# Performance work log

Measured on AMD Instinct MI355X. Metric: run time of the kernel, lower is better.

## Reference

```python
import jax, jax.numpy as jnp
import numpy as np

E = 1024   # embedding_dim
A = 1024   # attention_dim
H = 16     # num_heads
D = A // H # head_dim


def setup_inputs() -> dict:
    key = jax.random.key(0)
    ks = jax.random.split(key, 9)
    s = 1.0 / np.sqrt(E)
    so = 1.0 / np.sqrt(A)
    return {
        "x": jax.random.normal(ks[0], (2, 2048, E), dtype=jnp.float32),
        "Wq": jax.random.uniform(ks[1], (E, A), jnp.float32, -s, s),
        "bq": jax.random.uniform(ks[2], (A,), jnp.float32, -s, s),
        "Wk": jax.random.uniform(ks[3], (E, A), jnp.float32, -s, s),
        "bk": jax.random.uniform(ks[4], (A,), jnp.float32, -s, s),
        "Wv": jax.random.uniform(ks[5], (E, A), jnp.float32, -s, s),
        "bv": jax.random.uniform(ks[6], (A,), jnp.float32, -s, s),
        "Wo": jax.random.uniform(ks[7], (A, E), jnp.float32, -so, so),
        "bo": jax.random.uniform(ks[8], (E,), jnp.float32, -so, so),
    }


def reference(x, Wq, bq, Wk, bk, Wv, bv, Wo, bo):
    B, S, _ = x.shape
    # projections -> [B, H, S, D]
    def split_heads(t):
        return t.reshape(B, S, H, D).transpose(0, 2, 1, 3)
    Q = split_heads(x @ Wq + bq)
    K = split_heads(x @ Wk + bk)
    V = split_heads(x @ Wv + bv)
    scores = jnp.einsum("bhqd,bhkd->bhqk", Q, K) / jnp.sqrt(jnp.float32(D))
    causal = jnp.tril(jnp.ones((S, S), dtype=bool))
    scores = jnp.where(causal, scores, -jnp.inf)
    attn = jax.nn.softmax(scores, axis=-1)  # dropout p=0 (eval/deterministic)
    ctx = jnp.einsum("bhqk,bhkd->bhqd", attn, V)
    ctx = ctx.transpose(0, 2, 1, 3).reshape(B, S, A)
    out = ctx @ Wo + bo
    return (out, attn)
```

## Files before the change

### kernel.cpp

```cpp
#include <hip/hip_runtime.h>
#include <cstddef>

typedef __bf16 bf16_t;
typedef __attribute__((ext_vector_type(8))) __bf16 bf16x8;
typedef __attribute__((ext_vector_type(4))) float f32x4;

#define BATCH 2
#define SEQ   2048
#define EMB   1024
#define ADIM  1024
#define NHEAD 16
#define HDIM  64
#define MROWS 4096

__device__ inline unsigned short f2bf(float f) {
    bf16_t b = (bf16_t)f;
    return __builtin_bit_cast(unsigned short, b);
}

__global__ __launch_bounds__(256) void convert_x_kernel(
    const float* __restrict__ in, unsigned short* __restrict__ out, int n8)
{
    int i = blockIdx.x * 256 + threadIdx.x;
    if (i >= n8) return;
    const float4* p = (const float4*)(in + (size_t)i * 8);
    float4 a = p[0], b = p[1];
    unsigned int w0 = f2bf(a.x) | ((unsigned)f2bf(a.y) << 16);
    unsigned int w1 = f2bf(a.z) | ((unsigned)f2bf(a.w) << 16);
    unsigned int w2 = f2bf(b.x) | ((unsigned)f2bf(b.y) << 16);
    unsigned int w3 = f2bf(b.z) | ((unsigned)f2bf(b.w) << 16);
    uint4 v = {w0, w1, w2, w3};
    *(uint4*)(out + (size_t)i * 8) = v;
}

__global__ __launch_bounds__(256) void transpose_w_kernel(
    const float* __restrict__ Wq, const float* __restrict__ Wk,
    const float* __restrict__ Wv, const float* __restrict__ Wo,
    unsigned short* __restrict__ Wt_qkv, unsigned short* __restrict__ Wt_o)
{
    __shared__ float tile[64][65];
    const int m = blockIdx.z;
    const float* W = (m == 0) ? Wq : (m == 1) ? Wk : (m == 2) ? Wv : Wo;
    unsigned short* dst = (m < 3) ? (Wt_qkv + (size_t)m * 1024 * 1024) : Wt_o;
    const int r0 = blockIdx.y * 64, c0 = blockIdx.x * 64;
    const int t = threadIdx.x;
    const int r = t >> 2, c4 = (t & 3) * 16;
    #pragma unroll
    for (int j = 0; j < 16; j += 4) {
        float4 v = *(const float4*)(W + (size_t)(r0 + r) * 1024 + c0 + c4 + j);
        tile[r][c4 + j + 0] = v.x;
        tile[r][c4 + j + 1] = v.y;
        tile[r][c4 + j + 2] = v.z;
        tile[r][c4 + j + 3] = v.w;
    }
    __syncthreads();
    const int oc = t >> 2, ch = (t & 3) * 16;
    unsigned int ww[8];
    #pragma unroll
    for (int j = 0; j < 16; j += 2)
        ww[j >> 1] = f2bf(tile[ch + j][oc]) | ((unsigned)f2bf(tile[ch + j + 1][oc]) << 16);
    unsigned short* o = dst + (size_t)(c0 + oc) * 1024 + r0 + ch;
    *(uint4*)(o) = *(uint4*)&ww[0];
    *(uint4*)(o + 8) = *(uint4*)&ww[4];
}

template<int EPI>
__global__ __launch_bounds__(256) void gemm_mfma_kernel(
    const unsigned short* __restrict__ A,
    const unsigned short* __restrict__ Bt,
    const float* __restrict__ b0, const float* __restrict__ b1, const float* __restrict__ b2,
    void* __restrict__ outp, unsigned short* __restrict__ vt)
{
    __shared__ __align__(16) unsigned short Asm[4096];
    __shared__ __align__(16) unsigned short Bsm[4096];
    const int tid = threadIdx.x, lane = tid & 63, w = tid >> 6;
    const int wr = w >> 1, wc = w & 1;
    const int rowBase = blockIdx.y * 128, colBase = blockIdx.x * 128;
    const int K = 1024;

    f32x4 acc[4][4];
    #pragma unroll
    for (int i = 0; i < 4; ++i)
        #pragma unroll
        for (int j = 0; j < 4; ++j)
            acc[i][j] = (f32x4){0.f, 0.f, 0.f, 0.f};

    int mt_s[2], cc_s[2], r16_s[2];
    #pragma unroll
    for (int i = 0; i < 2; ++i) {
        int chunk = w * 128 + i * 64 + lane;
        mt_s[i] = chunk >> 6;
        cc_s[i] = (chunk & 63) >> 4;
        r16_s[i] = chunk & 15;
    }

    for (int k0 = 0; k0 < K; k0 += 32) {
        __syncthreads();
        #pragma unroll
        for (int i = 0; i < 2; ++i) {
            const unsigned short* ga = A + (size_t)(rowBase + mt_s[i] * 16 + r16_s[i]) * K + k0 + cc_s[i] * 8;
            __builtin_amdgcn_global_load_lds(
                (const __attribute__((address_space(1))) unsigned int*)ga,
                (__attribute__((address_space(3))) unsigned int*)(Asm + (size_t)(w * 128 + i * 64) * 8),
                16, 0, 0);
            const unsigned short* gb = Bt + (size_t)(colBase + mt_s[i] * 16 + r16_s[i]) * K + k0 + cc_s[i] * 8;
            __builtin_amdgcn_global_load_lds(
                (const __attribute__((address_space(1))) unsigned int*)gb,
                (__attribute__((address_space(3))) unsigned int*)(Bsm + (size_t)(w * 128 + i * 64) * 8),
                16, 0, 0);
        }
        __syncthreads();

        bf16x8 af[4], bfr[4];
        #pragma unroll
        for (int mt = 0; mt < 4; ++mt)
            af[mt] = *(const bf16x8*)(Asm + (size_t)((wr * 4 + mt) * 64 + lane) * 8);
        #pragma unroll
        for (int nt = 0; nt < 4; ++nt)
            bfr[nt] = *(const bf16x8*)(Bsm + (size_t)((wc * 4 + nt) * 64 + lane) * 8);
        #pragma unroll
        for (int mt = 0; mt < 4; ++mt)
            #pragma unroll
            for (int nt = 0; nt < 4; ++nt)
                acc[mt][nt] = __builtin_amdgcn_mfma_f32_16x16x32_bf16(af[mt], bfr[nt], acc[mt][nt], 0, 0, 0);
    }

    const int g = lane >> 4, r16 = lane & 15;
    const int seg = colBase >> 10;
    const float* bias = (seg == 0) ? b0 : (seg == 1) ? b1 : b2;

    if (EPI == 0) {
        unsigned short* qkv = (unsigned short*)outp;
        #pragma unroll
        for (int mt = 0; mt < 4; ++mt) {
            const int row0 = rowBase + wr * 64 + mt * 16 + 4 * g;
            #pragma unroll
            for (int nt = 0; nt < 4; ++nt) {
                const int col = colBase + wc * 64 + nt * 16 + r16;
                const float bb = bias[col & 1023];
                if (seg < 2) {
                    #pragma unroll
                    for (int rr = 0; rr < 4; ++rr)
                        qkv[(size_t)(row0 + rr) * 3072 + col] = f2bf(acc[mt][nt][rr] + bb);
                } else {
                    unsigned int p0 = f2bf(acc[mt][nt][0] + bb) | ((unsigned)f2bf(acc[mt][nt][1] + bb) << 16);
                    unsigned int p1 = f2bf(acc[mt][nt][2] + bb) | ((unsigned)f2bf(acc[mt][nt][3] + bb) << 16);
                    uint2 pv = {p0, p1};
                    *(uint2*)(vt + (size_t)(col - 2048) * 4096 + row0) = pv;
                }
            }
        }
    } else {
        float* out = (float*)outp;
        #pragma unroll
        for (int mt = 0; mt < 4; ++mt) {
            const int row0 = rowBase + wr * 64 + mt * 16 + 4 * g;
            #pragma unroll
            for (int nt = 0; nt < 4; ++nt) {
                const int col = colBase + wc * 64 + nt * 16 + r16;
                const float bb = bias[col];
                #pragma unroll
                for (int rr = 0; rr < 4; ++rr)
                    out[(size_t)(row0 + rr) * 1024 + col] = acc[mt][nt][rr] + bb;
            }
        }
    }
}

__global__ __launch_bounds__(256, 4) void attn_mfma_kernel(
    const unsigned short* __restrict__ qkv,
    const unsigned short* __restrict__ vt,
    float* __restrict__ attn,
    unsigned short* __restrict__ ctx)
{
    __shared__ __align__(16) unsigned short Ksm[2][4096];
    __shared__ __align__(16) unsigned short Vsm[2][4096];
    __shared__ __align__(16) unsigned short Psm[4][1024];

    const int j = blockIdx.x;
    const int xcd = j & 7, slot = j >> 3;
    const int bh = xcd + 8 * (slot & 3);
    const int s4 = slot >> 2;
    const int qt = 8 * (s4 >> 3) + (((s4 & 7) + 2 * (s4 >> 3)) & 7);
    const int b = bh >> 4, h = bh & 15;
    const int tid = threadIdx.x, lane = tid & 63, w = tid >> 6;
    const int g = lane >> 4, r16 = lane & 15;
    const int qrow0 = qt * 64 + w * 16;

    bf16x8 qf[2];
    #pragma unroll
    for (int k2 = 0; k2 < 2; ++k2)
        qf[k2] = *(const bf16x8*)(qkv + (size_t)(b * SEQ + qrow0 + r16) * 3072 + h * 64 + k2 * 32 + g * 8);

    const int sr = tid >> 2;
    const int sbc = (tid & 3) * 32;
    const int swz = (sr & 7) << 4;
    char* Kb = (char*)Ksm;
    char* Vb = (char*)Vsm;

    float rsum[4] = {0.f, 0.f, 0.f, 0.f};

    {
        const char* gk = (const char*)(qkv + (size_t)(b * SEQ + sr) * 3072 + 1024 + h * 64);
        uint4 a0 = *(const uint4*)(gk + sbc);
        uint4 a1 = *(const uint4*)(gk + sbc + 16);
        *(uint4*)(Kb + ((sr * 128 + sbc) ^ swz)) = a0;
        *(uint4*)(Kb + ((sr * 128 + sbc + 16) ^ swz)) = a1;
    }
    __syncthreads();
    for (int kt = 0; kt <= qt; ++kt) {
        const int cur = kt & 1;
        uint4 a0, a1;
        if (kt < qt) {
            const char* gk = (const char*)(qkv + (size_t)(b * SEQ + (kt + 1) * 64 + sr) * 3072 + 1024 + h * 64);
            a0 = *(const uint4*)(gk + sbc);
            a1 = *(const uint4*)(gk + sbc + 16);
        }
        const char* Kc = Kb + cur * 8192;
        #pragma unroll
        for (int nt = 0; nt < 4; ++nt) {
            f32x4 s = {0.f, 0.f, 0.f, 0.f};
            const int krow = nt * 16 + r16;
            #pragma unroll
            for (int k2 = 0; k2 < 2; ++k2) {
                bf16x8 kf = *(const bf16x8*)(Kc + ((krow * 128 + k2 * 64 + g * 16) ^ ((krow & 7) << 4)));
                s = __builtin_amdgcn_mfma_f32_16x16x32_bf16(qf[k2], kf, s, 0, 0, 0);
            }
            #pragma unroll
            for (int rr = 0; rr < 4; ++rr) {
                const int q = qrow0 + 4 * g + rr;
                const int k = kt * 64 + nt * 16 + r16;
                if (k <= q) rsum[rr] += __expf(s[rr] * 0.125f);
            }
        }
        if (kt < qt) {
            char* Kn = Kb + (cur ^ 1) * 8192;
            *(uint4*)(Kn + ((sr * 128 + sbc) ^ swz)) = a0;
            *(uint4*)(Kn + ((sr * 128 + sbc + 16) ^ swz)) = a1;
        }
        __syncthreads();
    }
    #pragma unroll
    for (int rr = 0; rr < 4; ++rr) {
        float v = rsum[rr];
        v += __shfl_xor(v, 1, 64);
        v += __shfl_xor(v, 2, 64);
        v += __shfl_xor(v, 4, 64);
        v += __shfl_xor(v, 8, 64);
        rsum[rr] = 1.0f / v;
    }

    f32x4 cacc[4];
    #pragma unroll
    for (int nt = 0; nt < 4; ++nt) cacc[nt] = (f32x4){0.f, 0.f, 0.f, 0.f};

    {
        const char* gk = (const char*)(qkv + (size_t)(b * SEQ + sr) * 3072 + 1024 + h * 64);
        uint4 a0 = *(const uint4*)(gk + sbc);
        uint4 a1 = *(const uint4*)(gk + sbc + 16);
        const char* gv = (const char*)(vt + (size_t)(h * 64 + sr) * 4096 + b * SEQ);
        uint4 v0 = *(const uint4*)(gv + sbc);
        uint4 v1 = *(const uint4*)(gv + sbc + 16);
        *(uint4*)(Kb + ((sr * 128 + sbc) ^ swz)) = a0;
        *(uint4*)(Kb + ((sr * 128 + sbc + 16) ^ swz)) = a1;
        *(uint4*)(Vb + ((sr * 128 + sbc) ^ swz)) = v0;
        *(uint4*)(Vb + ((sr * 128 + sbc + 16) ^ swz)) = v1;
    }
    __syncthreads();
    for (int kt = 0; kt <= qt; ++kt) {
        const int cur = kt & 1;
        const int kbase = kt * 64;
        uint4 a0, a1, v0, v1;
        if (kt < qt) {
            const char* gk = (const char*)(qkv + (size_t)(b * SEQ + kbase + 64 + sr) * 3072 + 1024 + h * 64);
            a0 = *(const uint4*)(gk + sbc);
            a1 = *(const uint4*)(gk + sbc + 16);
            const char* gv = (const char*)(vt + (size_t)(h * 64 + sr) * 4096 + b * SEQ + kbase + 64);
            v0 = *(const uint4*)(gv + sbc);
            v1 = *(const uint4*)(gv + sbc + 16);
        }
        const char* Kc = Kb + cur * 8192;
        const char* Vc = Vb + cur * 8192;

        #pragma unroll
        for (int nt = 0; nt < 4; ++nt) {
            f32x4 s = {0.f, 0.f, 0.f, 0.f};
            const int krow = nt * 16 + r16;
            #pragma unroll
            for (int k2 = 0; k2 < 2; ++k2) {
                bf16x8 kf = *(const bf16x8*)(Kc + ((krow * 128 + k2 * 64 + g * 16) ^ ((krow & 7) << 4)));
                s = __builtin_amdgcn_mfma_f32_16x16x32_bf16(qf[k2], kf, s, 0, 0, 0);
            }
            #pragma unroll
            for (int rr = 0; rr < 4; ++rr) {
                const int q = qrow0 + 4 * g + rr;
                const int k = kbase + nt * 16 + r16;
                float pn = 0.0f;
                if (k <= q) pn = __expf(s[rr] * 0.125f) * rsum[rr];
                attn[((size_t)bh * SEQ + q) * SEQ + k] = pn;
                const int prow = 4 * g + rr;
                *(unsigned short*)((char*)(Psm[w]) + ((prow * 128 + (nt * 16 + r16) * 2) ^ ((prow & 7) << 4))) = f2bf(pn);
            }
        }
        bf16x8 pf[2];
        #pragma unroll
        for (int k2 = 0; k2 < 2; ++k2)
            pf[k2] = *(const bf16x8*)((char*)(Psm[w]) + ((r16 * 128 + k2 * 64 + g * 16) ^ ((r16 & 7) << 4)));
        #pragma unroll
        for (int nt = 0; nt < 4; ++nt) {
            const int vrow = nt * 16 + r16;
            #pragma unroll
            for (int k2 = 0; k2 < 2; ++k2) {
                bf16x8 vf = *(const bf16x8*)(Vc + ((vrow * 128 + k2 * 64 + g * 16) ^ ((vrow & 7) << 4)));
                cacc[nt] = __builtin_amdgcn_mfma_f32_16x16x32_bf16(pf[k2], vf, cacc[nt], 0, 0, 0);
            }
        }
        if (kt < qt) {
            char* Kn = Kb + (cur ^ 1) * 8192;
            char* Vn = Vb + (cur ^ 1) * 8192;
            *(uint4*)(Kn + ((sr * 128 + sbc) ^ swz)) = a0;
            *(uint4*)(Kn + ((sr * 128 + sbc + 16) ^ swz)) = a1;
            *(uint4*)(Vn + ((sr * 128 + sbc) ^ swz)) = v0;
            *(uint4*)(Vn + ((sr * 128 + sbc + 16) ^ swz)) = v1;
        }
        __syncthreads();
    }

    #pragma unroll
    for (int nt = 0; nt < 4; ++nt)
        #pragma unroll
        for (int rr = 0; rr < 4; ++rr) {
            const int q = qrow0 + 4 * g + rr;
            ctx[(size_t)(b * SEQ + q) * 1024 + h * 64 + nt * 16 + r16] = f2bf(cacc[nt][rr]);
        }

    const int colStart = 64 * (qt + 1);
    const int Wc = SEQ - colStart;
    if (Wc > 0) {
        const int w4 = Wc >> 2;
        for (int c = tid; c < 64 * w4; c += 256) {
            const int row = qt * 64 + c / w4;
            const int col = colStart + (c % w4) * 4;
            *(float4*)(attn + ((size_t)bh * SEQ + row) * SEQ + col) = make_float4(0.f, 0.f, 0.f, 0.f);
        }
    }
}

extern "C" void kernel_launch(void* const* d_in, const int* in_sizes, int n_in,
                              void* d_out, int out_size, void* d_ws, size_t ws_size,
                              hipStream_t stream)
{
    const float* x  = (const float*)d_in[0];
    const float* Wq = (const float*)d_in[1];
    const float* bq = (const float*)d_in[2];
    const float* Wk = (const float*)d_in[3];
    const float* bk = (const float*)d_in[4];
    const float* Wv = (const float*)d_in[5];
    const float* bv = (const float*)d_in[6];
    const float* Wo = (const float*)d_in[7];
    const float* bo = (const float*)d_in[8];

    float* out  = (float*)d_out;
    float* attn = out + (size_t)BATCH * SEQ * EMB;

    unsigned short* xb     = (unsigned short*)d_ws;
    unsigned short* wt_qkv = xb + (size_t)MROWS * 1024;
    unsigned short* wt_o   = wt_qkv + (size_t)3072 * 1024;
    unsigned short* qkvb   = wt_o + (size_t)1024 * 1024;
    unsigned short* vtb    = qkvb + (size_t)MROWS * 3072;
    unsigned short* ctxb   = vtb + (size_t)1024 * MROWS;

    convert_x_kernel<<<2048, 256, 0, stream>>>(x, xb, MROWS * 1024 / 8);
    transpose_w_kernel<<<dim3(16, 16, 4), 256, 0, stream>>>(Wq, Wk, Wv, Wo, wt_qkv, wt_o);

    gemm_mfma_kernel<0><<<dim3(24, 32), 256, 0, stream>>>(xb, wt_qkv, bq, bk, bv, qkvb, vtb);

    attn_mfma_kernel<<<1024, 256, 0, stream>>>(qkvb, vtb, attn, ctxb);

    gemm_mfma_kernel<1><<<dim3(8, 32), 256, 0, stream>>>(ctxb, wt_o, bo, bo, bo, out, nullptr);
}
```

Baseline: 255.6 us.

## Peel diagonal tile, fold softmax scale into Q, batch MFMAs with setprio

```diff
diff --git a/kernel.cpp b/kernel.cpp
--- a/kernel.cpp
+++ b/kernel.cpp
@@ -131,6 +131,7 @@
 
     if (EPI == 0) {
         unsigned short* qkv = (unsigned short*)outp;
+        const float sc = (seg == 0) ? 0.125f : 1.0f;
         #pragma unroll
         for (int mt = 0; mt < 4; ++mt) {
             const int row0 = rowBase + wr * 64 + mt * 16 + 4 * g;
@@ -141,7 +142,7 @@
                 if (seg < 2) {
                     #pragma unroll
                     for (int rr = 0; rr < 4; ++rr)
-                        qkv[(size_t)(row0 + rr) * 3072 + col] = f2bf(acc[mt][nt][rr] + bb);
+                        qkv[(size_t)(row0 + rr) * 3072 + col] = f2bf((acc[mt][nt][rr] + bb) * sc);
                 } else {
                     unsigned int p0 = f2bf(acc[mt][nt][0] + bb) | ((unsigned)f2bf(acc[mt][nt][1] + bb) << 16);
                     unsigned int p1 = f2bf(acc[mt][nt][2] + bb) | ((unsigned)f2bf(acc[mt][nt][3] + bb) << 16);
@@ -208,37 +209,60 @@
         *(uint4*)(Kb + ((sr * 128 + sbc + 16) ^ swz)) = a1;
     }
     __syncthreads();
-    for (int kt = 0; kt <= qt; ++kt) {
+    for (int kt = 0; kt < qt; ++kt) {
         const int cur = kt & 1;
-        uint4 a0, a1;
-        if (kt < qt) {
-            const char* gk = (const char*)(qkv + (size_t)(b * SEQ + (kt + 1) * 64 + sr) * 3072 + 1024 + h * 64);
-            a0 = *(const uint4*)(gk + sbc);
-            a1 = *(const uint4*)(gk + sbc + 16);
-        }
+        const char* gk = (const char*)(qkv + (size_t)(b * SEQ + (kt + 1) * 64 + sr) * 3072 + 1024 + h * 64);
+        uint4 a0 = *(const uint4*)(gk + sbc);
+        uint4 a1 = *(const uint4*)(gk + sbc + 16);
         const char* Kc = Kb + cur * 8192;
-        #pragma unroll
-        for (int nt = 0; nt < 4; ++nt) {
-            f32x4 s = {0.f, 0.f, 0.f, 0.f};
+        f32x4 s[4];
+        #pragma unroll
+        for (int nt = 0; nt < 4; ++nt) s[nt] = (f32x4){0.f, 0.f, 0.f, 0.f};
+        __builtin_amdgcn_s_setprio(1);
+        #pragma unroll
+        for (int nt = 0; nt < 4; ++nt) {
             const int krow = nt * 16 + r16;
             #pragma unroll
             for (int k2 = 0; k2 < 2; ++k2) {
                 bf16x8 kf = *(const bf16x8*)(Kc + ((krow * 128 + k2 * 64 + g * 16) ^ ((krow & 7) << 4)));
-                s = __builtin_amdgcn_mfma_f32_16x16x32_bf16(qf[k2], kf, s, 0, 0, 0);
-            }
+                s[nt] = __builtin_amdgcn_mfma_f32_16x16x32_bf16(qf[k2], kf, s[nt], 0, 0, 0);
+            }
+        }
+        __builtin_amdgcn_s_setprio(0);
+        #pragma unroll
+        for (int nt = 0; nt < 4; ++nt)
+            #pragma unroll
+            for (int rr = 0; rr < 4; ++rr)
+                rsum[rr] += __expf(s[nt][rr]);
+        char* Kn = Kb + (cur ^ 1) * 8192;
+        *(uint4*)(Kn + ((sr * 128 + sbc) ^ swz)) = a0;
+        *(uint4*)(Kn + ((sr * 128 + sbc + 16) ^ swz)) = a1;
+        __syncthreads();
+    }
+    {
+        const char* Kc = Kb + (qt & 1) * 8192;
+        f32x4 s[4];
+        #pragma unroll
+        for (int nt = 0; nt < 4; ++nt) s[nt] = (f32x4){0.f, 0.f, 0.f, 0.f};
+        __builtin_amdgcn_s_setprio(1);
+        #pragma unroll
+        for (int nt = 0; nt < 4; ++nt) {
+            const int krow = nt * 16 + r16;
+            #pragma unroll
+            for (int k2 = 0; k2 < 2; ++k2) {
+                bf16x8 kf = *(const bf16x8*)(Kc + ((krow * 128 + k2 * 64 + g * 16) ^ ((krow & 7) << 4)));
+                s[nt] = __builtin_amdgcn_mfma_f32_16x16x32_bf16(qf[k2], kf, s[nt], 0, 0, 0);
+            }
+        }
+        __builtin_amdgcn_s_setprio(0);
+        #pragma unroll
+        for (int nt = 0; nt < 4; ++nt)
             #pragma unroll
             for (int rr = 0; rr < 4; ++rr) {
                 const int q = qrow0 + 4 * g + rr;
-                const int k = kt * 64 + nt * 16 + r16;
-                if (k <= q) rsum[rr] += __expf(s[rr] * 0.125f);
-            }
-        }
-        if (kt < qt) {
-            char* Kn = Kb + (cur ^ 1) * 8192;
-            *(uint4*)(Kn + ((sr * 128 + sbc) ^ swz)) = a0;
-            *(uint4*)(Kn + ((sr * 128 + sbc + 16) ^ swz)) = a1;
-        }
-        __syncthreads();
+                const int k = qt * 64 + nt * 16 + r16;
+                if (k <= q) rsum[rr] += __expf(s[nt][rr]);
+            }
     }
     #pragma unroll
     for (int rr = 0; rr < 4; ++rr) {
@@ -254,6 +278,8 @@
     #pragma unroll
     for (int nt = 0; nt < 4; ++nt) cacc[nt] = (f32x4){0.f, 0.f, 0.f, 0.f};
 
+    float* const abase = attn + ((size_t)bh * SEQ + qrow0 + 4 * g) * SEQ + r16;
+
     {
         const char* gk = (const char*)(qkv + (size_t)(b * SEQ + sr) * 3072 + 1024 + h * 64);
         uint4 a0 = *(const uint4*)(gk + sbc);
@@ -261,43 +287,102 @@
         const char* gv = (const char*)(vt + (size_t)(h * 64 + sr) * 4096 + b * SEQ);
         uint4 v0 = *(const uint4*)(gv + sbc);
         uint4 v1 = *(const uint4*)(gv + sbc + 16);
+        __syncthreads();
         *(uint4*)(Kb + ((sr * 128 + sbc) ^ swz)) = a0;
         *(uint4*)(Kb + ((sr * 128 + sbc + 16) ^ swz)) = a1;
         *(uint4*)(Vb + ((sr * 128 + sbc) ^ swz)) = v0;
         *(uint4*)(Vb + ((sr * 128 + sbc + 16) ^ swz)) = v1;
     }
     __syncthreads();
-    for (int kt = 0; kt <= qt; ++kt) {
+    for (int kt = 0; kt < qt; ++kt) {
         const int cur = kt & 1;
         const int kbase = kt * 64;
-        uint4 a0, a1, v0, v1;
-        if (kt < qt) {
-            const char* gk = (const char*)(qkv + (size_t)(b * SEQ + kbase + 64 + sr) * 3072 + 1024 + h * 64);
-            a0 = *(const uint4*)(gk + sbc);
-            a1 = *(const uint4*)(gk + sbc + 16);
-            const char* gv = (const char*)(vt + (size_t)(h * 64 + sr) * 4096 + b * SEQ + kbase + 64);
-            v0 = *(const uint4*)(gv + sbc);
-            v1 = *(const uint4*)(gv + sbc + 16);
-        }
+        const char* gk = (const char*)(qkv + (size_t)(b * SEQ + kbase + 64 + sr) * 3072 + 1024 + h * 64);
+        uint4 a0 = *(const uint4*)(gk + sbc);
+        uint4 a1 = *(const uint4*)(gk + sbc + 16);
+        const char* gv = (const char*)(vt + (size_t)(h * 64 + sr) * 4096 + b * SEQ + kbase + 64);
+        uint4 v0 = *(const uint4*)(gv + sbc);
+        uint4 v1 = *(const uint4*)(gv + sbc + 16);
         const char* Kc = Kb + cur * 8192;
         const char* Vc = Vb + cur * 8192;
 
-        #pragma unroll
-        for (int nt = 0; nt < 4; ++nt) {
-            f32x4 s = {0.f, 0.f, 0.f, 0.f};
+        f32x4 s[4];
+        #pragma unroll
+        for (int nt = 0; nt < 4; ++nt) s[nt] = (f32x4){0.f, 0.f, 0.f, 0.f};
+        __builtin_amdgcn_s_setprio(1);
+        #pragma unroll
+        for (int nt = 0; nt < 4; ++nt) {
             const int krow = nt * 16 + r16;
             #pragma unroll
             for (int k2 = 0; k2 < 2; ++k2) {
                 bf16x8 kf = *(const bf16x8*)(Kc + ((krow * 128 + k2 * 64 + g * 16) ^ ((krow & 7) << 4)));
-                s = __builtin_amdgcn_mfma_f32_16x16x32_bf16(qf[k2], kf, s, 0, 0, 0);
-            }
+                s[nt] = __builtin_amdgcn_mfma_f32_16x16x32_bf16(qf[k2], kf, s[nt], 0, 0, 0);
+            }
+        }
+        __builtin_amdgcn_s_setprio(0);
+
+        float* atile = abase + kbase;
+        #pragma unroll
+        for (int nt = 0; nt < 4; ++nt) {
+            #pragma unroll
+            for (int rr = 0; rr < 4; ++rr) {
+                const float pn = __expf(s[nt][rr]) * rsum[rr];
+                atile[(size_t)rr * SEQ + nt * 16] = pn;
+                const int prow = 4 * g + rr;
+                *(unsigned short*)((char*)(Psm[w]) + ((prow * 128 + (nt * 16 + r16) * 2) ^ ((prow & 7) << 4))) = f2bf(pn);
+            }
+        }
+        bf16x8 pf[2];
+        #pragma unroll
+        for (int k2 = 0; k2 < 2; ++k2)
+            pf[k2] = *(const bf16x8*)((char*)(Psm[w]) + ((r16 * 128 + k2 * 64 + g * 16) ^ ((r16 & 7) << 4)));
+        __builtin_amdgcn_s_setprio(1);
+        #pragma unroll
+        for (int nt = 0; nt < 4; ++nt) {
+            const int vrow = nt * 16 + r16;
+            #pragma unroll
+            for (int k2 = 0; k2 < 2; ++k2) {
+                bf16x8 vf = *(const bf16x8*)(Vc + ((vrow * 128 + k2 * 64 + g * 16) ^ ((vrow & 7) << 4)));
+                cacc[nt] = __builtin_amdgcn_mfma_f32_16x16x32_bf16(pf[k2], vf, cacc[nt], 0, 0, 0);
+            }
+        }
+        __builtin_amdgcn_s_setprio(0);
+        char* Kn = Kb + (cur ^ 1) * 8192;
+        char* Vn = Vb + (cur ^ 1) * 8192;
+        *(uint4*)(Kn + ((sr * 128 + sbc) ^ swz)) = a0;
+        *(uint4*)(Kn + ((sr * 128 + sbc + 16) ^ swz)) = a1;
+        *(uint4*)(Vn + ((sr * 128 + sbc) ^ swz)) = v0;
+        *(uint4*)(Vn + ((sr * 128 + sbc + 16) ^ swz)) = v1;
+        __syncthreads();
+    }
+    {
+        const int kbase = qt * 64;
+        const char* Kc = Kb + (qt & 1) * 8192;
+        const char* Vc = Vb + (qt & 1) * 8192;
+        f32x4 s[4];
+        #pragma unroll
+        for (int nt = 0; nt < 4; ++nt) s[nt] = (f32x4){0.f, 0.f, 0.f, 0.f};
+        __builtin_amdgcn_s_setprio(1);
+        #pragma unroll
+        for (int nt = 0; nt < 4; ++nt) {
+            const int krow = nt * 16 + r16;
+            #pragma unroll
+            for (int k2 = 0; k2 < 2; ++k2) {
+                bf16x8 kf = *(const bf16x8*)(Kc + ((krow * 128 + k2 * 64 + g * 16) ^ ((krow & 7) << 4)));
+                s[nt] = __builtin_amdgcn_mfma_f32_16x16x32_bf16(qf[k2], kf, s[nt], 0, 0, 0);
+            }
+        }
+        __builtin_amdgcn_s_setprio(0);
+        float* atile = abase + kbase;
+        #pragma unroll
+        for (int nt = 0; nt < 4; ++nt) {
             #pragma unroll
             for (int rr = 0; rr < 4; ++rr) {
                 const int q = qrow0 + 4 * g + rr;
                 const int k = kbase + nt * 16 + r16;
                 float pn = 0.0f;
-                if (k <= q) pn = __expf(s[rr] * 0.125f) * rsum[rr];
-                attn[((size_t)bh * SEQ + q) * SEQ + k] = pn;
+                if (k <= q) pn = __expf(s[nt][rr]) * rsum[rr];
+                atile[(size_t)rr * SEQ + nt * 16] = pn;
                 const int prow = 4 * g + rr;
                 *(unsigned short*)((char*)(Psm[w]) + ((prow * 128 + (nt * 16 + r16) * 2) ^ ((prow & 7) << 4))) = f2bf(pn);
             }
@@ -306,6 +391,7 @@
         #pragma unroll
         for (int k2 = 0; k2 < 2; ++k2)
             pf[k2] = *(const bf16x8*)((char*)(Psm[w]) + ((r16 * 128 + k2 * 64 + g * 16) ^ ((r16 & 7) << 4)));
+        __builtin_amdgcn_s_setprio(1);
         #pragma unroll
         for (int nt = 0; nt < 4; ++nt) {
             const int vrow = nt * 16 + r16;
@@ -315,15 +401,7 @@
                 cacc[nt] = __builtin_amdgcn_mfma_f32_16x16x32_bf16(pf[k2], vf, cacc[nt], 0, 0, 0);
             }
         }
-        if (kt < qt) {
-            char* Kn = Kb + (cur ^ 1) * 8192;
-            char* Vn = Vb + (cur ^ 1) * 8192;
-            *(uint4*)(Kn + ((sr * 128 + sbc) ^ swz)) = a0;
-            *(uint4*)(Kn + ((sr * 128 + sbc + 16) ^ swz)) = a1;
-            *(uint4*)(Vn + ((sr * 128 + sbc) ^ swz)) = v0;
-            *(uint4*)(Vn + ((sr * 128 + sbc + 16) ^ swz)) = v1;
-        }
-        __syncthreads();
+        __builtin_amdgcn_s_setprio(0);
     }
 
     #pragma unroll
```

Result: slower. 265.4 us (+3.9%).
